# Kernel optimization log

Hardware: AMD Instinct MI355X
Metric: run time of the kernel (lower is better)

The kernel has to match this reference:

```python
import jax, jax.numpy as jnp
import numpy as np


def _haar_kernel():
    # 8 orthonormal 3D Haar taps, order (zf,yf,xf) in {L,H}^3 -> subband index s=4*z+2*y+x
    s2 = np.sqrt(2.0)
    L = np.array([1.0, 1.0]) / s2
    H = np.array([1.0, -1.0]) / s2
    taps = []
    for zf in (L, H):
        for yf in (L, H):
            for xf in (L, H):
                taps.append(np.einsum('i,j,k->ijk', zf, yf, xf))
    return jnp.asarray(np.stack(taps, 0), dtype=jnp.float32)  # [8,2,2,2]


def setup_inputs() -> dict:
    key = jax.random.key(0)
    ks = jax.random.split(key, 9)
    C, mid = 128, 8  # channels=128, reduction=16 -> mid = max(1, 128//16)
    x = jax.random.normal(ks[0], (2, C, 64, 64, 64), jnp.float32)
    def p(k, shape):
        return jax.random.normal(k, shape, jnp.float32) * 0.05
    return {
        'x': x,
        'gw1': p(ks[1], (mid, C)), 'gb1': p(ks[2], (mid,)),
        'gw2': p(ks[3], (C, mid)), 'gb2': p(ks[4], (C,)),
        'lw1': p(ks[5], (mid, C)), 'lb1': p(ks[6], (mid,)),
        'lw2': p(ks[7], (C, mid)), 'lb2': p(ks[8], (C,)),
    }


def _mlp(t, w1, b1, w2, b2):
    # 1x1x1 Conv3d -> ReLU -> 1x1x1 Conv3d, t: [B,C,D,H,W]
    h = jnp.einsum('bcdhw,mc->bmdhw', t, w1) + b1[None, :, None, None, None]
    h = jax.nn.relu(h)
    return jnp.einsum('bmdhw,cm->bcdhw', h, w2) + b2[None, :, None, None, None]


def reference(x, gw1, gb1, gw2, gb2, lw1, lb1, lw2, lb2):
    k = _haar_kernel()  # [8,2,2,2]
    B, C, D, H, W = x.shape
    # depthwise stride-2 2x2x2 conv == non-overlapping block transform
    xr = x.reshape(B, C, D // 2, 2, H // 2, 2, W // 2, 2)
    y = jnp.einsum('bcdphqwr,spqr->bcsdhw', xr, k)  # [B,C,8,D/2,H/2,W/2]
    low = y[:, :, 0]        # [B,C,D/2,H/2,W/2]
    highs = y[:, :, 1:]     # [B,C,7,D/2,H/2,W/2]
    x_sum = low + highs.sum(axis=2)
    gap = x_sum.mean(axis=(2, 3, 4), keepdims=True)  # AdaptiveAvgPool3d(1)
    w = jax.nn.sigmoid(_mlp(gap, gw1, gb1, gw2, gb2) + _mlp(x_sum, lw1, lb1, lw2, lb2))
    y_mod = jnp.concatenate([low[:, :, None], highs * w[:, :, None]], axis=2)
    # conv_transpose of orthonormal Haar == inverse block transform
    xr2 = jnp.einsum('bcsdhw,spqr->bcdphqwr', y_mod, k)
    return xr2.reshape(B, C, D, H, W)
```

## Files before the change

### kernel.cpp

```cpp
#include <hip/hip_runtime.h>
#include <math.h>

#define C_ 128
#define MID 8
#define CS 262144
#define SQRT8 2.8284271247461903f

static __device__ __forceinline__ float sigmoidf_(float z) {
    return 1.0f / (1.0f + __expf(-z));
}

__global__ __launch_bounds__(256) void gap_partial_kernel(
    const float* __restrict__ x,
    float* __restrict__ partial)
{
    __shared__ float red[4];
    const int blk = blockIdx.x;
    const int g = blk & 7;
    const int c = (blk >> 3) & 127;
    const int b = blk >> 10;
    const int tid = threadIdx.x;
    const int f = tid & 15;

    const float* xb = x + (size_t)(b * C_ + c) * CS;
    float s = 0.0f;
    #pragma unroll
    for (int k = 0; k < 8; ++k) {
        const int r   = (tid >> 4) + 16 * k;
        const int dcl = r >> 5;
        const int hc  = r & 31;
        const float4 v = ((const float4*)(
            xb + (size_t)(2 * (4 * g + dcl)) * 4096 + (size_t)(2 * hc) * 64))[f];
        s += v.x + v.z;
    }
    s += __shfl_down(s, 32);
    s += __shfl_down(s, 16);
    s += __shfl_down(s, 8);
    s += __shfl_down(s, 4);
    s += __shfl_down(s, 2);
    s += __shfl_down(s, 1);
    if ((tid & 63) == 0) red[tid >> 6] = s;
    __syncthreads();
    if (tid == 0) partial[blk] = red[0] + red[1] + red[2] + red[3];
}

__global__ __launch_bounds__(256) void gmlp_kernel(
    const float* __restrict__ partial,
    const float* __restrict__ gw1, const float* __restrict__ gb1,
    const float* __restrict__ gw2, const float* __restrict__ gb2,
    const float* __restrict__ lb2,
    float* __restrict__ gbias)
{
    __shared__ float sgap[2][C_];
    __shared__ float shid[2][MID];
    const int t = threadIdx.x;
    const int b = t >> 7, c = t & 127;
    {
        const float4* p = (const float4*)(partial + (size_t)t * 8);
        const float4 a = p[0], d = p[1];
        sgap[b][c] = (a.x + a.y + a.z + a.w + d.x + d.y + d.z + d.w)
                     * (SQRT8 / 32768.0f);
    }
    __syncthreads();
    if (t < 16) {
        const int bb = t >> 3, m = t & 7;
        float a = gb1[m];
        for (int cc = 0; cc < C_; ++cc) a += gw1[m * C_ + cc] * sgap[bb][cc];
        shid[bb][m] = fmaxf(a, 0.0f);
    }
    __syncthreads();
    float a = gb2[c] + lb2[c];
    #pragma unroll
    for (int m = 0; m < MID; ++m) a += gw2[c * MID + m] * shid[b][m];
    gbias[t] = a;
}

__global__ __launch_bounds__(256) void fused_blend_kernel(
    const float* __restrict__ x,
    const float* __restrict__ lw1, const float* __restrict__ lb1,
    const float* __restrict__ lw2,
    const float* __restrict__ gbias,
    float* __restrict__ out)
{
    __shared__ float xs[C_ * 17];
    __shared__ float shid[MID * 16];
    __shared__ float s1T[C_ * MID];
    __shared__ float s2T[MID * C_];
    __shared__ float sgb[C_];

    const int blk = blockIdx.x;
    const int wh  = blk & 1;
    const int hc  = (blk >> 1) & 31;
    const int dc  = (blk >> 6) & 31;
    const int b   = blk >> 11;
    const int tid = threadIdx.x;
    const int f   = tid & 7;
    const int c0  = tid >> 3;

    for (int i = tid; i < MID * C_; i += 256) {
        s1T[i] = lw1[(i & 7) * C_ + (i >> 3)];
        s2T[i] = lw2[(i & 127) * MID + (i >> 7)];
    }
    if (tid < C_) sgb[tid] = gbias[b * C_ + tid];

    const float* xb = x + (size_t)b * C_ * CS
                    + (size_t)(2 * dc) * 4096 + (size_t)(2 * hc) * 64 + wh * 32;

    float4 r00[4];
    #pragma unroll
    for (int k = 0; k < 4; ++k) {
        const int c = c0 + 32 * k;
        const float4 v = ((const float4*)(xb + (size_t)c * CS))[f];
        r00[k] = v;
        xs[c * 17 + 2 * f]     = SQRT8 * v.x;
        xs[c * 17 + 2 * f + 1] = SQRT8 * v.z;
    }
    __syncthreads();

    if (tid < 128) {
        const int m = tid >> 4, wc = tid & 15;
        float a = lb1[m];
        for (int cc = 0; cc < C_; ++cc) a += s1T[cc * MID + m] * xs[cc * 17 + wc];
        shid[m * 16 + wc] = fmaxf(a, 0.0f);
    }
    __syncthreads();

    float* ob = out + (xb - x);
    #pragma unroll
    for (int k = 0; k < 4; ++k) {
        const int c = c0 + 32 * k;
        const size_t coff = (size_t)c * CS;

        const float4 a01 = ((const float4*)(xb + coff + 64))[f];
        const float4 a10 = ((const float4*)(xb + coff + 4096))[f];
        const float4 a11 = ((const float4*)(xb + coff + 4160))[f];
        const float4 a00 = r00[k];

        float d0 = sgb[c], d1 = sgb[c];
        #pragma unroll
        for (int m = 0; m < MID; ++m) {
            const float wv = s2T[m * C_ + c];
            d0 += wv * shid[m * 16 + 2 * f];
            d1 += wv * shid[m * 16 + 2 * f + 1];
        }
        const float w0 = sigmoidf_(d0);
        const float w1 = sigmoidf_(d1);

        const float mean0 = (a00.x + a00.y + a01.x + a01.y +
                             a10.x + a10.y + a11.x + a11.y) * 0.125f;
        const float mean1 = (a00.z + a00.w + a01.z + a01.w +
                             a10.z + a10.w + a11.z + a11.w) * 0.125f;
        const float om0 = (1.0f - w0) * mean0;
        const float om1 = (1.0f - w1) * mean1;

        float4 o;
        o.x = w0 * a00.x + om0; o.y = w0 * a00.y + om0;
        o.z = w1 * a00.z + om1; o.w = w1 * a00.w + om1;
        ((float4*)(ob + coff))[f] = o;
        o.x = w0 * a01.x + om0; o.y = w0 * a01.y + om0;
        o.z = w1 * a01.z + om1; o.w = w1 * a01.w + om1;
        ((float4*)(ob + coff + 64))[f] = o;
        o.x = w0 * a10.x + om0; o.y = w0 * a10.y + om0;
        o.z = w1 * a10.z + om1; o.w = w1 * a10.w + om1;
        ((float4*)(ob + coff + 4096))[f] = o;
        o.x = w0 * a11.x + om0; o.y = w0 * a11.y + om0;
        o.z = w1 * a11.z + om1; o.w = w1 * a11.w + om1;
        ((float4*)(ob + coff + 4160))[f] = o;
    }
}

extern "C" void kernel_launch(void* const* d_in, const int* in_sizes, int n_in,
                              void* d_out, int out_size, void* d_ws, size_t ws_size,
                              hipStream_t stream) {
    const float* x   = (const float*)d_in[0];
    const float* gw1 = (const float*)d_in[1];
    const float* gb1 = (const float*)d_in[2];
    const float* gw2 = (const float*)d_in[3];
    const float* gb2 = (const float*)d_in[4];
    const float* lw1 = (const float*)d_in[5];
    const float* lb1 = (const float*)d_in[6];
    const float* lw2 = (const float*)d_in[7];
    const float* lb2 = (const float*)d_in[8];
    float* o  = (float*)d_out;
    float* ws = (float*)d_ws;

    float* partial = ws;
    float* gbias   = ws + 2048;

    gap_partial_kernel<<<2048, 256, 0, stream>>>(x, partial);
    gmlp_kernel<<<1, 256, 0, stream>>>(partial, gw1, gb1, gw2, gb2, lb2, gbias);
    fused_blend_kernel<<<4096, 256, 0, stream>>>(x, lw1, lb1, lw2, gbias, o);
}
```

Before: 480.7 us.

## Fuse global MLP into GAP via last-block atomic, prefetch and nontemporal blend IO

```diff
diff --git a/kernel.cpp b/kernel.cpp
--- a/kernel.cpp
+++ b/kernel.cpp
@@ -5,16 +5,28 @@
 #define MID 8
 #define CS 262144
 #define SQRT8 2.8284271247461903f
+#define NBLK_GAP 2048
+
+typedef float vf4 __attribute__((ext_vector_type(4)));
 
 static __device__ __forceinline__ float sigmoidf_(float z) {
     return 1.0f / (1.0f + __expf(-z));
 }
 
-__global__ __launch_bounds__(256) void gap_partial_kernel(
+__global__ __launch_bounds__(256) void gap_kernel(
     const float* __restrict__ x,
-    float* __restrict__ partial)
+    const float* __restrict__ gw1, const float* __restrict__ gb1,
+    const float* __restrict__ gw2, const float* __restrict__ gb2,
+    const float* __restrict__ lb2,
+    float* __restrict__ partial,
+    unsigned int* __restrict__ done,
+    float* __restrict__ gbias)
 {
     __shared__ float red[4];
+    __shared__ int amLast;
+    __shared__ float sgap[2][C_];
+    __shared__ float shid[2][MID];
+
     const int blk = blockIdx.x;
     const int g = blk & 7;
     const int c = (blk >> 3) & 127;
@@ -29,7 +41,7 @@
         const int r   = (tid >> 4) + 16 * k;
         const int dcl = r >> 5;
         const int hc  = r & 31;
-        const float4 v = ((const float4*)(
+        const vf4 v = ((const vf4*)(
             xb + (size_t)(2 * (4 * g + dcl)) * 4096 + (size_t)(2 * hc) * 64))[f];
         s += v.x + v.z;
     }
@@ -41,37 +53,38 @@
     s += __shfl_down(s, 1);
     if ((tid & 63) == 0) red[tid >> 6] = s;
     __syncthreads();
-    if (tid == 0) partial[blk] = red[0] + red[1] + red[2] + red[3];
-}
-
-__global__ __launch_bounds__(256) void gmlp_kernel(
-    const float* __restrict__ partial,
-    const float* __restrict__ gw1, const float* __restrict__ gb1,
-    const float* __restrict__ gw2, const float* __restrict__ gb2,
-    const float* __restrict__ lb2,
-    float* __restrict__ gbias)
-{
-    __shared__ float sgap[2][C_];
-    __shared__ float shid[2][MID];
-    const int t = threadIdx.x;
-    const int b = t >> 7, c = t & 127;
+    if (tid == 0) {
+        const float v = red[0] + red[1] + red[2] + red[3];
+        __hip_atomic_store(&partial[blk], v, __ATOMIC_RELEASE,
+                           __HIP_MEMORY_SCOPE_AGENT);
+        const unsigned int prev = __hip_atomic_fetch_add(
+            done, 1u, __ATOMIC_ACQ_REL, __HIP_MEMORY_SCOPE_AGENT);
+        amLast = (prev == NBLK_GAP - 1);
+    }
+    __syncthreads();
+    if (!amLast) return;
+
+    const int t = tid;
+    const int bb = t >> 7, cc = t & 127;
     {
-        const float4* p = (const float4*)(partial + (size_t)t * 8);
-        const float4 a = p[0], d = p[1];
-        sgap[b][c] = (a.x + a.y + a.z + a.w + d.x + d.y + d.z + d.w)
-                     * (SQRT8 / 32768.0f);
+        float tot = 0.0f;
+        #pragma unroll
+        for (int j = 0; j < 8; ++j)
+            tot += __hip_atomic_load(&partial[(size_t)t * 8 + j],
+                                     __ATOMIC_RELAXED, __HIP_MEMORY_SCOPE_AGENT);
+        sgap[bb][cc] = tot * (SQRT8 / 32768.0f);
     }
     __syncthreads();
     if (t < 16) {
-        const int bb = t >> 3, m = t & 7;
+        const int b2 = t >> 3, m = t & 7;
         float a = gb1[m];
-        for (int cc = 0; cc < C_; ++cc) a += gw1[m * C_ + cc] * sgap[bb][cc];
-        shid[bb][m] = fmaxf(a, 0.0f);
-    }
-    __syncthreads();
-    float a = gb2[c] + lb2[c];
-    #pragma unroll
-    for (int m = 0; m < MID; ++m) a += gw2[c * MID + m] * shid[b][m];
+        for (int k = 0; k < C_; ++k) a += gw1[m * C_ + k] * sgap[b2][k];
+        shid[b2][m] = fmaxf(a, 0.0f);
+    }
+    __syncthreads();
+    float a = gb2[cc] + lb2[cc];
+    #pragma unroll
+    for (int m = 0; m < MID; ++m) a += gw2[cc * MID + m] * shid[bb][m];
     gbias[t] = a;
 }
 
@@ -106,15 +119,21 @@
     const float* xb = x + (size_t)b * C_ * CS
                     + (size_t)(2 * dc) * 4096 + (size_t)(2 * hc) * 64 + wh * 32;
 
-    float4 r00[4];
+    vf4 r00[4];
     #pragma unroll
     for (int k = 0; k < 4; ++k) {
         const int c = c0 + 32 * k;
-        const float4 v = ((const float4*)(xb + (size_t)c * CS))[f];
+        const vf4 v = ((const vf4*)(xb + (size_t)c * CS))[f];
         r00[k] = v;
         xs[c * 17 + 2 * f]     = SQRT8 * v.x;
         xs[c * 17 + 2 * f + 1] = SQRT8 * v.z;
     }
+
+    const size_t coff0 = (size_t)c0 * CS;
+    vf4 p01 = __builtin_nontemporal_load((const vf4*)(xb + coff0 + 64) + f);
+    vf4 p10 = __builtin_nontemporal_load((const vf4*)(xb + coff0 + 4096) + f);
+    vf4 p11 = __builtin_nontemporal_load((const vf4*)(xb + coff0 + 4160) + f);
+
     __syncthreads();
 
     if (tid < 128) {
@@ -131,10 +150,17 @@
         const int c = c0 + 32 * k;
         const size_t coff = (size_t)c * CS;
 
-        const float4 a01 = ((const float4*)(xb + coff + 64))[f];
-        const float4 a10 = ((const float4*)(xb + coff + 4096))[f];
-        const float4 a11 = ((const float4*)(xb + coff + 4160))[f];
-        const float4 a00 = r00[k];
+        const vf4 a00 = r00[k];
+        const vf4 a01 = p01;
+        const vf4 a10 = p10;
+        const vf4 a11 = p11;
+
+        if (k < 3) {
+            const size_t cn = (size_t)(c + 32) * CS;
+            p01 = __builtin_nontemporal_load((const vf4*)(xb + cn + 64) + f);
+            p10 = __builtin_nontemporal_load((const vf4*)(xb + cn + 4096) + f);
+            p11 = __builtin_nontemporal_load((const vf4*)(xb + cn + 4160) + f);
+        }
 
         float d0 = sgb[c], d1 = sgb[c];
         #pragma unroll
@@ -153,19 +179,19 @@
         const float om0 = (1.0f - w0) * mean0;
         const float om1 = (1.0f - w1) * mean1;
 
-        float4 o;
+        vf4 o;
         o.x = w0 * a00.x + om0; o.y = w0 * a00.y + om0;
         o.z = w1 * a00.z + om1; o.w = w1 * a00.w + om1;
-        ((float4*)(ob + coff))[f] = o;
+        __builtin_nontemporal_store(o, (vf4*)(ob + coff) + f);
         o.x = w0 * a01.x + om0; o.y = w0 * a01.y + om0;
         o.z = w1 * a01.z + om1; o.w = w1 * a01.w + om1;
-        ((float4*)(ob + coff + 64))[f] = o;
+        __builtin_nontemporal_store(o, (vf4*)(ob + coff + 64) + f);
         o.x = w0 * a10.x + om0; o.y = w0 * a10.y + om0;
         o.z = w1 * a10.z + om1; o.w = w1 * a10.w + om1;
-        ((float4*)(ob + coff + 4096))[f] = o;
+        __builtin_nontemporal_store(o, (vf4*)(ob + coff + 4096) + f);
         o.x = w0 * a11.x + om0; o.y = w0 * a11.y + om0;
         o.z = w1 * a11.z + om1; o.w = w1 * a11.w + om1;
-        ((float4*)(ob + coff + 4160))[f] = o;
+        __builtin_nontemporal_store(o, (vf4*)(ob + coff + 4160) + f);
     }
 }
 
@@ -184,10 +210,12 @@
     float* o  = (float*)d_out;
     float* ws = (float*)d_ws;
 
-    float* partial = ws;
-    float* gbias   = ws + 2048;
-
-    gap_partial_kernel<<<2048, 256, 0, stream>>>(x, partial);
-    gmlp_kernel<<<1, 256, 0, stream>>>(partial, gw1, gb1, gw2, gb2, lb2, gbias);
+    float* partial     = ws;
+    float* gbias       = ws + 2048;
+    unsigned int* done = (unsigned int*)(ws + 2304);
+
+    (void)hipMemsetAsync(done, 0, sizeof(unsigned int), stream);
+    gap_kernel<<<NBLK_GAP, 256, 0, stream>>>(x, gw1, gb1, gw2, gb2, lb2,
+                                             partial, done, gbias);
     fused_blend_kernel<<<4096, 256, 0, stream>>>(x, lw1, lb1, lw2, gbias, o);
 }
```

Result: slower. 620.5 us (+29.1%).
